# Kernel tuning notes

Measured on AMD Instinct MI355X. Metric: run time of the kernel, lower is better.

The kernel has to match this reference:

```python
import jax, jax.numpy as jnp
import numpy as np

B, N, C, H = 8, 1024, 768, 12
D = C // H          # head_dim = 64
M = 2 * D           # rand_feat_dim = 128
SCALE = D ** -0.5
EPS = 1e-12         # F.normalize eps


def _feature_map(z, rand_matrix):
    # z: [B,H,N,D] already multiplied by sqrt(scale); proj: [H,D,M]
    logits = jnp.einsum('bhnd,hdm->bhnm', z, rand_matrix)
    sqnorm = 0.5 * jnp.sum(z * z, axis=-1, keepdims=True)
    return jnp.exp(logits - sqnorm) * (M ** -0.5)


def setup_inputs() -> dict:
    key = jax.random.key(0)
    k1, k2, k3, k4, k5 = jax.random.split(key, 5)
    x = jax.random.normal(k1, (B, N, C), dtype=jnp.float32)
    qkv_w = jax.random.normal(k2, (3 * C, C), dtype=jnp.float32) * 0.02
    proj_w = jax.random.normal(k3, (C, C), dtype=jnp.float32) * 0.02
    proj_b = jax.random.normal(k4, (C,), dtype=jnp.float32) * 0.02
    rand_matrix = jax.random.normal(k5, (H, D, M), dtype=jnp.float32)
    return {"x": x, "qkv_w": qkv_w, "proj_w": proj_w, "proj_b": proj_b,
            "rand_matrix": rand_matrix}


def reference(x, qkv_w, proj_w, proj_b, rand_matrix):
    b, n, c = x.shape
    # qkv projection (torch Linear, no bias): [B,N,3C] -> [3,B,H,N,D]
    qkv = (x @ qkv_w.T).reshape(b, n, 3, H, D).transpose(2, 0, 3, 1, 4)
    q, k, v = qkv[0], qkv[1], qkv[2]
    sq = SCALE ** 0.5
    qf = _feature_map(q * sq, rand_matrix)   # [B,H,N,M]
    kf = _feature_map(k * sq, rand_matrix)   # [B,H,N,M]
    attn = jnp.einsum('bhnm,bhkm->bhnk', qf, kf)          # explicit O(N^2)
    denom = jnp.maximum(jnp.sum(jnp.abs(attn), axis=-1, keepdims=True), EPS)
    attn = attn / denom                                   # L1 normalize
    out = jnp.einsum('bhnk,bhkd->bhnd', attn, v)          # [B,H,N,D]
    out = out.transpose(0, 2, 1, 3).reshape(b, n, c)
    return out @ proj_w.T + proj_b
```

## Files before the change

kernel.cpp:

```cpp
#include <hip/hip_runtime.h>
#include <hip/hip_bf16.h>

#define PB 8
#define PN 1024
#define PC 768
#define PH 12
#define PD 64
#define PM 128
#define SQ 0.35355339059327373f
#define MSCALE 0.08838834764831843f

typedef _Float16 f16;
typedef f16 f16x8 __attribute__((ext_vector_type(8)));
typedef f16 f16x4 __attribute__((ext_vector_type(4)));
typedef float f32x4 __attribute__((ext_vector_type(4)));

#define GLL(src, dst) __builtin_amdgcn_global_load_lds( \
    (const __attribute__((address_space(1))) void*)(src), \
    (__attribute__((address_space(3))) void*)(dst), 16, 0, 0)

__global__ __launch_bounds__(192) void conv_all(
        const float* __restrict__ x, const float* __restrict__ qkv_w,
        const float* __restrict__ proj_w, const float* __restrict__ rm,
        f16* __restrict__ Ax, f16* __restrict__ Bqk, f16* __restrict__ Bp,
        f16* __restrict__ Rt)
{
    const int bid = blockIdx.x;
    const int t = threadIdx.x;
    if (bid < 11264) {
        const float* src; f16* dst; int r;
        if (bid < 8192)       { src = x;      dst = Ax;  r = bid; }
        else if (bid < 10496) { src = qkv_w;  dst = Bqk; r = bid - 8192; }
        else                  { src = proj_w; dst = Bp;  r = bid - 10496; }
        const int c = t * 4;
        float4 v = *(const float4*)&src[(size_t)r * PC + c];
        f16x4 hv;
        hv.x = (f16)v.x; hv.y = (f16)v.y; hv.z = (f16)v.z; hv.w = (f16)v.w;
        *(f16x4*)&dst[(size_t)r * PC + c] = hv;
    } else {
        const int h = bid - 11264;
        for (int e = t; e < PD * PM; e += 192)
            Rt[(size_t)h * 8192 + e] = (f16)rm[(size_t)h * 8192 + (e & 63) * PM + (e >> 6)];
    }
}

__global__ __launch_bounds__(256) void gemm_qkv(
        const f16* __restrict__ A,
        const f16* __restrict__ Bm,
        f16* __restrict__ zq, f16* __restrict__ zk, f16* __restrict__ vh,
        float* __restrict__ sqq, float* __restrict__ sqk)
{
    __shared__ f16 As[128 * 64];
    __shared__ f16 Bs[128 * 64];
    const int t = threadIdx.x;
    const int wave = t >> 6, lane = t & 63;
    const int wm = wave >> 1, wn = wave & 1;
    const int bi = blockIdx.y * 128, bj = blockIdx.x * 128;

    f32x4 acc[4][4] = {};

    const int rowi = lane >> 3;
    const int cb = (lane & 7) ^ ((lane >> 4) & 3);
    const f16* ApE = A + (size_t)(bi + wave * 32 + rowi) * PC + cb * 8;
    const f16* ApO = A + (size_t)(bi + wave * 32 + rowi) * PC + (cb ^ 4) * 8;
    const f16* BpE = Bm + (size_t)(bj + wave * 32 + rowi) * PC + cb * 8;
    const f16* BpO = Bm + (size_t)(bj + wave * 32 + rowi) * PC + (cb ^ 4) * 8;
    f16* AsB = &As[wave * 32 * 64];
    f16* BsB = &Bs[wave * 32 * 64];

    const int q4 = lane >> 4;
    for (int kt = 0; kt < 12; ++kt) {
        const int k0 = kt * 64;
        __syncthreads();
        GLL(ApE + k0,               AsB);
        GLL(ApO + k0 + (size_t) 8 * PC, AsB + 8 * 64);
        GLL(ApE + k0 + (size_t)16 * PC, AsB + 16 * 64);
        GLL(ApO + k0 + (size_t)24 * PC, AsB + 24 * 64);
        GLL(BpE + k0,               BsB);
        GLL(BpO + k0 + (size_t) 8 * PC, BsB + 8 * 64);
        GLL(BpE + k0 + (size_t)16 * PC, BsB + 16 * 64);
        GLL(BpO + k0 + (size_t)24 * PC, BsB + 24 * 64);
        __syncthreads();

        #pragma unroll
        for (int kh = 0; kh < 2; ++kh) {
            f16x8 af[4], bf[4];
            #pragma unroll
            for (int i = 0; i < 4; ++i) {
                const int r = wm * 64 + i * 16 + (lane & 15);
                const int p = (kh * 4 + q4) ^ ((r >> 1) & 7);
                af[i] = *(const f16x8*)&As[r * 64 + p * 8];
            }
            #pragma unroll
            for (int j = 0; j < 4; ++j) {
                const int r = wn * 64 + j * 16 + (lane & 15);
                const int p = (kh * 4 + q4) ^ ((r >> 1) & 7);
                bf[j] = *(const f16x8*)&Bs[r * 64 + p * 8];
            }
            #pragma unroll
            for (int i = 0; i < 4; ++i)
                #pragma unroll
                for (int j = 0; j < 4; ++j)
                    acc[i][j] = __builtin_amdgcn_mfma_f32_16x16x32_f16(af[i], bf[j], acc[i][j], 0, 0, 0);
        }
    }

    const int quad = lane >> 4, cc = lane & 15;
    const int colbase = bj + wn * 64;
    const int b = bi >> 10;
    if (colbase < 1536) {
        const int which = colbase >= 768;
        const int h = (colbase - which * 768) >> 6;
        f16* zdst = which ? zk : zq;
        float* sdst = which ? sqk : sqq;
        const size_t bh = (size_t)(b * PH + h);
        #pragma unroll
        for (int i = 0; i < 4; ++i) {
            const int row0 = bi + wm * 64 + i * 16 + quad * 4;
            #pragma unroll
            for (int r = 0; r < 4; ++r) {
                const int n = (row0 + r) & 1023;
                f16 zh[4]; float psq = 0.f;
                #pragma unroll
                for (int j = 0; j < 4; ++j) {
                    zh[j] = (f16)(acc[i][j][r] * SQ);
                    float zf = (float)zh[j];
                    psq += zf * zf;
                }
                psq += __shfl_xor(psq, 1, 64);
                psq += __shfl_xor(psq, 2, 64);
                psq += __shfl_xor(psq, 4, 64);
                psq += __shfl_xor(psq, 8, 64);
                if (cc == 0) sdst[(bh << 10) + n] = 0.5f * psq;
                f16* zp = zdst + (((bh << 10) + n) << 6);
                #pragma unroll
                for (int j = 0; j < 4; ++j) zp[j * 16 + cc] = zh[j];
            }
        }
    } else {
        const int h = (colbase - 1536) >> 6;
        const size_t bh = (size_t)(b * PH + h);
        #pragma unroll
        for (int i = 0; i < 4; ++i) {
            const int row0 = bi + wm * 64 + i * 16 + quad * 4;
            #pragma unroll
            for (int r = 0; r < 4; ++r) {
                const int n = (row0 + r) & 1023;
                f16* vp = vh + (((bh << 10) + n) << 6);
                #pragma unroll
                for (int j = 0; j < 4; ++j) vp[j * 16 + cc] = (f16)acc[i][j][r];
            }
        }
    }
}

__global__ __launch_bounds__(256) void feat_kv(
        const f16* __restrict__ zk, const f16* __restrict__ Rt,
        const float* __restrict__ sqk, const f16* __restrict__ vh,
        float* __restrict__ kvp, float* __restrict__ sbufp)
{
    __shared__ __align__(16) char smem[52224];
    f16* As = (f16*)smem;
    f16* Bs = (f16*)(smem + 16384);
    f16* Pt = (f16*)smem;
    f16* vT = (f16*)(smem + 34816);
    __shared__ float sqs[128];

    const int t = threadIdx.x;
    const int wave = t >> 6, lane = t & 63;
    const int wm = wave >> 1, wn = wave & 1;
    const int nt = blockIdx.x, bh = blockIdx.y;
    const int h = bh % PH;

    const f16* A = zk + (((size_t)bh << 10) + nt * 128) * 64;
    const f16* Bm = Rt + (size_t)h * (PM * PD);

    if (t < 128) sqs[t] = sqk[((size_t)bh << 10) + nt * 128 + t];

    const int rowi = lane >> 3;
    const int cb = (lane & 7) ^ ((lane >> 4) & 3);
    const f16* ApE = A + (size_t)(wave * 32 + rowi) * 64 + cb * 8;
    const f16* ApO = A + (size_t)(wave * 32 + rowi) * 64 + (cb ^ 4) * 8;
    const f16* BpE = Bm + (size_t)(wave * 32 + rowi) * 64 + cb * 8;
    const f16* BpO = Bm + (size_t)(wave * 32 + rowi) * 64 + (cb ^ 4) * 8;
    f16* AsB = &As[wave * 32 * 64];
    f16* BsB = &Bs[wave * 32 * 64];
    GLL(ApE,            AsB);
    GLL(ApO + 8 * 64,   AsB + 8 * 64);
    GLL(ApE + 16 * 64,  AsB + 16 * 64);
    GLL(ApO + 24 * 64,  AsB + 24 * 64);
    GLL(BpE,            BsB);
    GLL(BpO + 8 * 64,   BsB + 8 * 64);
    GLL(BpE + 16 * 64,  BsB + 16 * 64);
    GLL(BpO + 24 * 64,  BsB + 24 * 64);
    __syncthreads();

    const int q4 = lane >> 4;
    f32x4 acc[4][4] = {};
    #pragma unroll
    for (int kh = 0; kh < 2; ++kh) {
        f16x8 af[4], bf[4];
        #pragma unroll
        for (int i = 0; i < 4; ++i) {
            const int r = wm * 64 + i * 16 + (lane & 15);
            const int p = (kh * 4 + q4) ^ ((r >> 1) & 7);
            af[i] = *(const f16x8*)&As[r * 64 + p * 8];
        }
        #pragma unroll
        for (int j = 0; j < 4; ++j) {
            const int r = wn * 64 + j * 16 + (lane & 15);
            const int p = (kh * 4 + q4) ^ ((r >> 1) & 7);
            bf[j] = *(const f16x8*)&Bs[r * 64 + p * 8];
        }
        #pragma unroll
        for (int i = 0; i < 4; ++i)
            #pragma unroll
            for (int j = 0; j < 4; ++j)
                acc[i][j] = __builtin_amdgcn_mfma_f32_16x16x32_f16(af[i], bf[j], acc[i][j], 0, 0, 0);
    }

    const int quad = lane >> 4, cc = lane & 15;
    __syncthreads();

    #pragma unroll
    for (int i = 0; i < 4; ++i) {
        #pragma unroll
        for (int j = 0; j < 4; ++j) {
            const int col = wn * 64 + j * 16 + cc;
            #pragma unroll
            for (int r = 0; r < 4; ++r) {
                const int rl = wm * 64 + i * 16 + quad * 4 + r;
                Pt[col * 136 + rl] = (f16)(__expf(acc[i][j][r] - sqs[rl]) * MSCALE);
            }
        }
    }
    {
        const int vn = t >> 1;
        const int vhf = (t & 1) * 32;
        const f16* vbase = vh + (((size_t)bh << 10) + nt * 128 + vn) * 64 + vhf;
        #pragma unroll
        for (int k = 0; k < 4; ++k) {
            f16x8 vv = *(const f16x8*)&vbase[k * 8];
            #pragma unroll
            for (int e = 0; e < 8; ++e)
                vT[(vhf + k * 8 + e) * 136 + vn] = vv[e];
        }
    }
    __syncthreads();

    f32x4 acc2[4][2] = {};
    #pragma unroll
    for (int kt = 0; kt < 4; ++kt) {
        const int kb = kt * 32 + (lane >> 4) * 8;
        f16x8 af2[4], bf2[2];
        #pragma unroll
        for (int i = 0; i < 4; ++i)
            af2[i] = *(const f16x8*)&Pt[(wm * 64 + i * 16 + (lane & 15)) * 136 + kb];
        #pragma unroll
        for (int j = 0; j < 2; ++j)
            bf2[j] = *(const f16x8*)&vT[(wn * 32 + j * 16 + (lane & 15)) * 136 + kb];
        #pragma unroll
        for (int i = 0; i < 4; ++i)
            #pragma unroll
            for (int j = 0; j < 2; ++j)
                acc2[i][j] = __builtin_amdgcn_mfma_f32_16x16x32_f16(af2[i], bf2[j], acc2[i][j], 0, 0, 0);
    }

    float* kvo = kvp + (size_t)(nt * 96 + bh) * 8192;
    #pragma unroll
    for (int i = 0; i < 4; ++i) {
        #pragma unroll
        for (int j = 0; j < 2; ++j) {
            const int d = wn * 32 + j * 16 + cc;
            #pragma unroll
            for (int r = 0; r < 4; ++r) {
                const int m = wm * 64 + i * 16 + quad * 4 + r;
                kvo[m * 64 + d] = acc2[i][j][r];
            }
        }
    }
    {
        const int sm = t >> 1, shf = (t & 1) * 64;
        float sp = 0.f;
        #pragma unroll
        for (int k = 0; k < 8; ++k) {
            f16x8 pv = *(const f16x8*)&Pt[sm * 136 + shf + k * 8];
            #pragma unroll
            for (int e = 0; e < 8; ++e) sp += (float)pv[e];
        }
        sp += __shfl_xor(sp, 1, 64);
        if ((t & 1) == 0) sbufp[(size_t)(nt * 96 + bh) * 128 + sm] = sp;
    }
}

__global__ __launch_bounds__(256) void kv_reduce(
        const float* __restrict__ kvp, const float* __restrict__ sbufp,
        float* __restrict__ kv, float* __restrict__ s)
{
    const int idx = blockIdx.x * 256 + threadIdx.x;
    float a = 0.f;
    #pragma unroll
    for (int c = 0; c < 8; ++c) a += kvp[(size_t)c * 786432 + idx];
    kv[idx] = a;
    if (idx < 96 * PM) {
        float sa = 0.f;
        #pragma unroll
        for (int c = 0; c < 8; ++c) sa += sbufp[(size_t)c * 96 * PM + idx];
        s[idx] = sa;
    }
}

__global__ __launch_bounds__(256) void feat_apply(
        const f16* __restrict__ zq, const f16* __restrict__ Rt,
        const float* __restrict__ sqq, const float* __restrict__ kvf,
        const float* __restrict__ sf, f16* __restrict__ ohA)
{
    __shared__ __align__(16) char smem[52224];
    f16* As = (f16*)smem;
    f16* Bs = (f16*)(smem + 16384);
    f16* Pn = (f16*)smem;
    f16* kvT = (f16*)(smem + 34816);
    __shared__ float sqs[128], ssm[128], dns[128];

    const int t = threadIdx.x;
    const int wave = t >> 6, lane = t & 63;
    const int wm = wave >> 1, wn = wave & 1;
    const int nt = blockIdx.x, bh = blockIdx.y;
    const int b = bh / PH, h = bh % PH;

    const f16* A = zq + (((size_t)bh << 10) + nt * 128) * 64;
    const f16* Bm = Rt + (size_t)h * (PM * PD);

    if (t < 128) {
        sqs[t] = sqq[((size_t)bh << 10) + nt * 128 + t];
        ssm[t] = sf[(size_t)bh * 128 + t];
    }

    const int rowi = lane >> 3;
    const int cb = (lane & 7) ^ ((lane >> 4) & 3);
    const f16* ApE = A + (size_t)(wave * 32 + rowi) * 64 + cb * 8;
    const f16* ApO = A + (size_t)(wave * 32 + rowi) * 64 + (cb ^ 4) * 8;
    const f16* BpE = Bm + (size_t)(wave * 32 + rowi) * 64 + cb * 8;
    const f16* BpO = Bm + (size_t)(wave * 32 + rowi) * 64 + (cb ^ 4) * 8;
    f16* AsB = &As[wave * 32 * 64];
    f16* BsB = &Bs[wave * 32 * 64];
    GLL(ApE,            AsB);
    GLL(ApO + 8 * 64,   AsB + 8 * 64);
    GLL(ApE + 16 * 64,  AsB + 16 * 64);
    GLL(ApO + 24 * 64,  AsB + 24 * 64);
    GLL(BpE,            BsB);
    GLL(BpO + 8 * 64,   BsB + 8 * 64);
    GLL(BpE + 16 * 64,  BsB + 16 * 64);
    GLL(BpO + 24 * 64,  BsB + 24 * 64);
    __syncthreads();

    const int q4 = lane >> 4;
    f32x4 acc[4][4] = {};
    #pragma unroll
    for (int kh = 0; kh < 2; ++kh) {
        f16x8 af[4], bf[4];
        #pragma unroll
        for (int i = 0; i < 4; ++i) {
            const int r = wm * 64 + i * 16 + (lane & 15);
            const int p = (kh * 4 + q4) ^ ((r >> 1) & 7);
            af[i] = *(const f16x8*)&As[r * 64 + p * 8];
        }
        #pragma unroll
        for (int j = 0; j < 4; ++j) {
            const int r = wn * 64 + j * 16 + (lane & 15);
            const int p = (kh * 4 + q4) ^ ((r >> 1) & 7);
            bf[j] = *(const f16x8*)&Bs[r * 64 + p * 8];
        }
        #pragma unroll
        for (int i = 0; i < 4; ++i)
            #pragma unroll
            for (int j = 0; j < 4; ++j)
                acc[i][j] = __builtin_amdgcn_mfma_f32_16x16x32_f16(af[i], bf[j], acc[i][j], 0, 0, 0);
    }

    const int quad = lane >> 4, cc = lane & 15;
    __syncthreads();

    #pragma unroll
    for (int i = 0; i < 4; ++i) {
        #pragma unroll
        for (int j = 0; j < 4; ++j) {
            const int col = wn * 64 + j * 16 + cc;
            #pragma unroll
            for (int r = 0; r < 4; ++r) {
                const int rl = wm * 64 + i * 16 + quad * 4 + r;
                Pn[rl * 136 + col] = (f16)(__expf(acc[i][j][r] - sqs[rl]) * MSCALE);
            }
        }
    }
    {
        const int m = t >> 1;
        const int dh2 = (t & 1) * 32;
        const float* kvb = kvf + ((size_t)bh * 128 + m) * 64 + dh2;
        #pragma unroll
        for (int k = 0; k < 8; ++k) {
            float4 k4 = *(const float4*)&kvb[k * 4];
            kvT[(dh2 + k * 4 + 0) * 136 + m] = (f16)k4.x;
            kvT[(dh2 + k * 4 + 1) * 136 + m] = (f16)k4.y;
            kvT[(dh2 + k * 4 + 2) * 136 + m] = (f16)k4.z;
            kvT[(dh2 + k * 4 + 3) * 136 + m] = (f16)k4.w;
        }
    }
    __syncthreads();

    {
        const int n = t >> 1, mh = (t & 1) * 64;
        float p = 0.f;
        #pragma unroll
        for (int k = 0; k < 8; ++k) {
            f16x8 pv = *(const f16x8*)&Pn[n * 136 + mh + k * 8];
            #pragma unroll
            for (int e = 0; e < 8; ++e)
                p += (float)pv[e] * ssm[mh + k * 8 + e];
        }
        p += __shfl_xor(p, 1, 64);
        if ((t & 1) == 0) dns[n] = (p < 1e-12f) ? 1e-12f : p;
    }
    __syncthreads();

    f32x4 acc3[4][2] = {};
    #pragma unroll
    for (int kt = 0; kt < 4; ++kt) {
        const int kb = kt * 32 + (lane >> 4) * 8;
        f16x8 af3[4], bf3[2];
        #pragma unroll
        for (int i = 0; i < 4; ++i)
            af3[i] = *(const f16x8*)&Pn[(wm * 64 + i * 16 + (lane & 15)) * 136 + kb];
        #pragma unroll
        for (int j = 0; j < 2; ++j)
            bf3[j] = *(const f16x8*)&kvT[(wn * 32 + j * 16 + (lane & 15)) * 136 + kb];
        #pragma unroll
        for (int i = 0; i < 4; ++i)
            #pragma unroll
            for (int j = 0; j < 2; ++j)
                acc3[i][j] = __builtin_amdgcn_mfma_f32_16x16x32_f16(af3[i], bf3[j], acc3[i][j], 0, 0, 0);
    }

    f16* ob = ohA + ((size_t)(b * PN) + nt * 128) * PC + h * PD;
    #pragma unroll
    for (int i = 0; i < 4; ++i) {
        #pragma unroll
        for (int j = 0; j < 2; ++j) {
            const int d = wn * 32 + j * 16 + cc;
            #pragma unroll
            for (int r = 0; r < 4; ++r) {
                const int n = wm * 64 + i * 16 + quad * 4 + r;
                ob[(size_t)n * PC + d] = (f16)(acc3[i][j][r] / dns[n]);
            }
        }
    }
}

__global__ __launch_bounds__(256) void gemm_proj(
        const f16* __restrict__ A,
        const f16* __restrict__ Bm,
        float* __restrict__ Cm, const float* __restrict__ bias)
{
    __shared__ f16 As[128 * 64];
    __shared__ f16 Bs[64 * 64];
    const int t = threadIdx.x;
    const int wave = t >> 6, lane = t & 63;
    const int wm = wave >> 1, wn = wave & 1;
    const int bi = blockIdx.y * 128, bj = blockIdx.x * 64;

    f32x4 acc[4][2] = {};

    const int rowi = lane >> 3;
    const int cb = (lane & 7) ^ ((lane >> 4) & 3);
    const f16* ApE = A + (size_t)(bi + wave * 32 + rowi) * PC + cb * 8;
    const f16* ApO = A + (size_t)(bi + wave * 32 + rowi) * PC + (cb ^ 4) * 8;
    const f16* BpE = Bm + (size_t)(bj + wave * 16 + rowi) * PC + cb * 8;
    const f16* BpO = Bm + (size_t)(bj + wave * 16 + rowi) * PC + (cb ^ 4) * 8;
    f16* AsB = &As[wave * 32 * 64];
    f16* BsB = &Bs[wave * 16 * 64];

    const int q4 = lane >> 4;
    for (int kt = 0; kt < 12; ++kt) {
        const int k0 = kt * 64;
        __syncthreads();
        GLL(ApE + k0,               AsB);
        GLL(ApO + k0 + (size_t) 8 * PC, AsB + 8 * 64);
        GLL(ApE + k0 + (size_t)16 * PC, AsB + 16 * 64);
        GLL(ApO + k0 + (size_t)24 * PC, AsB + 24 * 64);
        GLL(BpE + k0,               BsB);
        GLL(BpO + k0 + (size_t) 8 * PC, BsB + 8 * 64);
        __syncthreads();

        #pragma unroll
        for (int kh = 0; kh < 2; ++kh) {
            f16x8 af[4], bf[2];
            #pragma unroll
            for (int i = 0; i < 4; ++i) {
                const int r = wm * 64 + i * 16 + (lane & 15);
                const int p = (kh * 4 + q4) ^ ((r >> 1) & 7);
                af[i] = *(const f16x8*)&As[r * 64 + p * 8];
            }
            #pragma unroll
            for (int j = 0; j < 2; ++j) {
                const int r = wn * 32 + j * 16 + (lane & 15);
                const int p = (kh * 4 + q4) ^ ((r >> 1) & 7);
                bf[j] = *(const f16x8*)&Bs[r * 64 + p * 8];
            }
            #pragma unroll
            for (int i = 0; i < 4; ++i)
                #pragma unroll
                for (int j = 0; j < 2; ++j)
                    acc[i][j] = __builtin_amdgcn_mfma_f32_16x16x32_f16(af[i], bf[j], acc[i][j], 0, 0, 0);
        }
    }

    const int cr = (lane >> 4) * 4, cc = lane & 15;
    #pragma unroll
    for (int i = 0; i < 4; ++i) {
        const int row = bi + wm * 64 + i * 16 + cr;
        #pragma unroll
        for (int j = 0; j < 2; ++j) {
            const int col = bj + wn * 32 + j * 16 + cc;
            const float bv = bias[col];
            #pragma unroll
            for (int r = 0; r < 4; ++r)
                Cm[(size_t)(row + r) * PC + col] = acc[i][j][r] + bv;
        }
    }
}

extern "C" void kernel_launch(void* const* d_in, const int* in_sizes, int n_in,
                              void* d_out, int out_size, void* d_ws, size_t ws_size,
                              hipStream_t stream) {
    const float* x      = (const float*)d_in[0];
    const float* qkv_w  = (const float*)d_in[1];
    const float* proj_w = (const float*)d_in[2];
    const float* proj_b = (const float*)d_in[3];
    const float* rm     = (const float*)d_in[4];
    float* out = (float*)d_out;

    char* ws = (char*)d_ws;
    f16*   Ax   = (f16*)(ws);
    f16*   Bqk  = (f16*)(ws + 12582912);
    f16*   Bp   = (f16*)(ws + 16121856);
    f16*   Rt   = (f16*)(ws + 17301504);
    f16*   zq   = (f16*)(ws + 17498112);
    f16*   zk   = (f16*)(ws + 30081024);
    f16*   vh   = (f16*)(ws + 42663936);
    float* sqq  = (float*)(ws + 55246848);
    float* sqk  = (float*)(ws + 55640064);
    float* sbufp= (float*)(ws + 56033280);
    float* kvf  = (float*)(ws + 56426496);
    float* sf   = (float*)(ws + 59572224);
    f16*   ohA  = (f16*)(ws + 59621376);
    float* kvp = (float*)d_out;

    conv_all<<<11276, 192, 0, stream>>>(x, qkv_w, proj_w, rm, Ax, Bqk, Bp, Rt);

    gemm_qkv<<<dim3(18, 64), 256, 0, stream>>>(Ax, Bqk, zq, zk, vh, sqq, sqk);

    feat_kv<<<dim3(8, 96), 256, 0, stream>>>(zk, Rt, sqk, vh, kvp, sbufp);
    kv_reduce<<<3072, 256, 0, stream>>>(kvp, sbufp, kvf, sf);

    feat_apply<<<dim3(8, 96), 256, 0, stream>>>(zq, Rt, sqq, kvf, sf, ohA);

    gemm_proj<<<dim3(12, 64), 256, 0, stream>>>(ohA, Bp, out, proj_b);
}
```

Before: 189.5 us.

## Replace kv partial-sum reduction kernel with atomics and swap GEMM grid order

The partial KV and normalizer sums from feat_kv are now accumulated directly into the final buffers with float atomicAdd. Those buffers are zeroed by extra blocks in the conversion kernel, which lets the separate kv_reduce launch and its partial-sum traffic be removed. GEMM grids are also transposed so consecutive blocks walk along rows of A instead of columns of B, which changes cache reuse order. Atomics add contention, since 8 blocks hit each element, and make the summation order nondeterministic.

```diff
diff --git a/kernel.cpp b/kernel.cpp
--- a/kernel.cpp
+++ b/kernel.cpp
@@ -23,7 +23,7 @@
         const float* __restrict__ x, const float* __restrict__ qkv_w,
         const float* __restrict__ proj_w, const float* __restrict__ rm,
         f16* __restrict__ Ax, f16* __restrict__ Bqk, f16* __restrict__ Bp,
-        f16* __restrict__ Rt)
+        f16* __restrict__ Rt, float* __restrict__ kvf, float* __restrict__ sf)
 {
     const int bid = blockIdx.x;
     const int t = threadIdx.x;
@@ -37,10 +37,16 @@
         f16x4 hv;
         hv.x = (f16)v.x; hv.y = (f16)v.y; hv.z = (f16)v.z; hv.w = (f16)v.w;
         *(f16x4*)&dst[(size_t)r * PC + c] = hv;
-    } else {
+    } else if (bid < 11276) {
         const int h = bid - 11264;
         for (int e = t; e < PD * PM; e += 192)
             Rt[(size_t)h * 8192 + e] = (f16)rm[(size_t)h * 8192 + (e & 63) * PM + (e >> 6)];
+    } else if (bid < 12300) {
+        float4 z = make_float4(0.f, 0.f, 0.f, 0.f);
+        *(float4*)&kvf[(size_t)(bid - 11276) * 768 + t * 4] = z;
+    } else {
+        float4 z = make_float4(0.f, 0.f, 0.f, 0.f);
+        *(float4*)&sf[(size_t)(bid - 12300) * 768 + t * 4] = z;
     }
 }
 
@@ -55,7 +61,7 @@
     const int t = threadIdx.x;
     const int wave = t >> 6, lane = t & 63;
     const int wm = wave >> 1, wn = wave & 1;
-    const int bi = blockIdx.y * 128, bj = blockIdx.x * 128;
+    const int bi = blockIdx.x * 128, bj = blockIdx.y * 128;
 
     f32x4 acc[4][4] = {};
 
@@ -157,7 +163,7 @@
 __global__ __launch_bounds__(256) void feat_kv(
         const f16* __restrict__ zk, const f16* __restrict__ Rt,
         const float* __restrict__ sqk, const f16* __restrict__ vh,
-        float* __restrict__ kvp, float* __restrict__ sbufp)
+        float* __restrict__ kvf, float* __restrict__ sf)
 {
     __shared__ __align__(16) char smem[52224];
     f16* As = (f16*)smem;
@@ -266,7 +272,7 @@
                 acc2[i][j] = __builtin_amdgcn_mfma_f32_16x16x32_f16(af2[i], bf2[j], acc2[i][j], 0, 0, 0);
     }
 
-    float* kvo = kvp + (size_t)(nt * 96 + bh) * 8192;
+    float* kvo = kvf + (size_t)bh * 8192;
     #pragma unroll
     for (int i = 0; i < 4; ++i) {
         #pragma unroll
@@ -275,7 +281,7 @@
             #pragma unroll
             for (int r = 0; r < 4; ++r) {
                 const int m = wm * 64 + i * 16 + quad * 4 + r;
-                kvo[m * 64 + d] = acc2[i][j][r];
+                atomicAdd(&kvo[m * 64 + d], acc2[i][j][r]);
             }
         }
     }
@@ -289,24 +295,7 @@
             for (int e = 0; e < 8; ++e) sp += (float)pv[e];
         }
         sp += __shfl_xor(sp, 1, 64);
-        if ((t & 1) == 0) sbufp[(size_t)(nt * 96 + bh) * 128 + sm] = sp;
-    }
-}
-
-__global__ __launch_bounds__(256) void kv_reduce(
-        const float* __restrict__ kvp, const float* __restrict__ sbufp,
-        float* __restrict__ kv, float* __restrict__ s)
-{
-    const int idx = blockIdx.x * 256 + threadIdx.x;
-    float a = 0.f;
-    #pragma unroll
-    for (int c = 0; c < 8; ++c) a += kvp[(size_t)c * 786432 + idx];
-    kv[idx] = a;
-    if (idx < 96 * PM) {
-        float sa = 0.f;
-        #pragma unroll
-        for (int c = 0; c < 8; ++c) sa += sbufp[(size_t)c * 96 * PM + idx];
-        s[idx] = sa;
+        if ((t & 1) == 0) atomicAdd(&sf[(size_t)bh * 128 + sm], sp);
     }
 }
 
@@ -466,7 +455,7 @@
     const int t = threadIdx.x;
     const int wave = t >> 6, lane = t & 63;
     const int wm = wave >> 1, wn = wave & 1;
-    const int bi = blockIdx.y * 128, bj = blockIdx.x * 64;
+    const int bi = blockIdx.x * 128, bj = blockIdx.y * 64;
 
     f32x4 acc[4][2] = {};
 
@@ -549,20 +538,17 @@
     f16*   vh   = (f16*)(ws + 42663936);
     float* sqq  = (float*)(ws + 55246848);
     float* sqk  = (float*)(ws + 55640064);
-    float* sbufp= (float*)(ws + 56033280);
-    float* kvf  = (float*)(ws + 56426496);
-    float* sf   = (float*)(ws + 59572224);
-    f16*   ohA  = (f16*)(ws + 59621376);
-    float* kvp = (float*)d_out;
-
-    conv_all<<<11276, 192, 0, stream>>>(x, qkv_w, proj_w, rm, Ax, Bqk, Bp, Rt);
-
-    gemm_qkv<<<dim3(18, 64), 256, 0, stream>>>(Ax, Bqk, zq, zk, vh, sqq, sqk);
-
-    feat_kv<<<dim3(8, 96), 256, 0, stream>>>(zk, Rt, sqk, vh, kvp, sbufp);
-    kv_reduce<<<3072, 256, 0, stream>>>(kvp, sbufp, kvf, sf);
+    float* kvf  = (float*)(ws + 56033280);
+    float* sf   = (float*)(ws + 59179008);
+    f16*   ohA  = (f16*)(ws + 59228160);
+
+    conv_all<<<12316, 192, 0, stream>>>(x, qkv_w, proj_w, rm, Ax, Bqk, Bp, Rt, kvf, sf);
+
+    gemm_qkv<<<dim3(64, 18), 256, 0, stream>>>(Ax, Bqk, zq, zk, vh, sqq, sqk);
+
+    feat_kv<<<dim3(8, 96), 256, 0, stream>>>(zk, Rt, sqk, vh, kvf, sf);
 
     feat_apply<<<dim3(8, 96), 256, 0, stream>>>(zq, Rt, sqq, kvf, sf, ohA);
 
-    gemm_proj<<<dim3(12, 64), 256, 0, stream>>>(ohA, Bp, out, proj_b);
+    gemm_proj<<<dim3(64, 12), 256, 0, stream>>>(ohA, Bp, out, proj_b);
 }
```

Result: no change. 187.5 us (-1.1%).
